# Performance work log

Measured on AMD Instinct MI355X. Metric: run time of the kernel, lower is better.

The kernel has to match this reference:

```python
import jax, jax.numpy as jnp
import numpy as np

B, BARS, BEATS, FRAC = 64, 16, 4, 8
IN_F = 10 * 47 * 2  # 940
LIN_OUT = 100
BEAT_H = 16
BAR_H = 32


def _p(key, shape, scale=0.05):
    return jax.random.normal(key, shape, dtype=jnp.float32) * scale


def setup_inputs() -> dict:
    key = jax.random.key(0)
    ks = jax.random.split(key, 16)
    return {
        "channels": jax.random.normal(ks[0], (B, BARS, BEATS, FRAC, 10, 2, 47), dtype=jnp.float32),
        "lin_w": _p(ks[1], (LIN_OUT, IN_F)),
        "lin_b": _p(ks[2], (LIN_OUT,)),
        # beats LSTM (unidirectional), PyTorch gate order i,f,g,o
        "b_wih": _p(ks[3], (4 * BEAT_H, LIN_OUT)),
        "b_whh": _p(ks[4], (4 * BEAT_H, BEAT_H)),
        "b_bih": _p(ks[5], (4 * BEAT_H,)),
        "b_bhh": _p(ks[6], (4 * BEAT_H,)),
        # bars LSTM, bidirectional: forward (f_) and reverse (r_) directions
        "f_wih": _p(ks[7], (4 * BAR_H, BEAT_H)),
        "f_whh": _p(ks[8], (4 * BAR_H, BAR_H)),
        "f_bih": _p(ks[9], (4 * BAR_H,)),
        "f_bhh": _p(ks[10], (4 * BAR_H,)),
        "r_wih": _p(ks[11], (4 * BAR_H, BEAT_H)),
        "r_whh": _p(ks[12], (4 * BAR_H, BAR_H)),
        "r_bih": _p(ks[13], (4 * BAR_H,)),
        "r_bhh": _p(ks[14], (4 * BAR_H,)),
    }


def lstm(x, wih, whh, bih, bhh):
    """PyTorch-semantics LSTM, batch_first. x: [N, T, F] -> h_seq [N, T, H]."""
    N = x.shape[0]
    H = whh.shape[1]
    # precompute input contribution for all timesteps
    xg = jnp.einsum('ntf,gf->ntg', x, wih) + (bih + bhh)  # [N, T, 4H]

    def step(carry, xt):
        h, c = carry
        gates = xt + h @ whh.T  # [N, 4H]
        i, f, g, o = jnp.split(gates, 4, axis=-1)
        c = jax.nn.sigmoid(f) * c + jax.nn.sigmoid(i) * jnp.tanh(g)
        h = jax.nn.sigmoid(o) * jnp.tanh(c)
        return (h, c), h

    h0 = jnp.zeros((N, H), x.dtype)
    _, hs = jax.lax.scan(step, (h0, h0), jnp.swapaxes(xg, 0, 1))  # [T, N, H]
    return jnp.swapaxes(hs, 0, 1)


def bilstm(x, f_wih, f_whh, f_bih, f_bhh, r_wih, r_whh, r_bih, r_bhh):
    fwd = lstm(x, f_wih, f_whh, f_bih, f_bhh)
    bwd = jnp.flip(lstm(jnp.flip(x, axis=1), r_wih, r_whh, r_bih, r_bhh), axis=1)
    return jnp.concatenate([fwd, bwd], axis=-1)


def reference(channels, lin_w, lin_b,
              b_wih, b_whh, b_bih, b_bhh,
              f_wih, f_whh, f_bih, f_bhh,
              r_wih, r_whh, r_bih, r_bhh):
    # channels: [B, bars, beats, frac, 10, 2, 47]
    x = jnp.swapaxes(channels, -1, -2)  # [..., 10, 47, 2]
    x = x.reshape(*x.shape[:4], IN_F)   # squash dims 4..6 -> 940
    x = jax.nn.relu(x @ lin_w.T + lin_b)  # [B, bars, beats, frac, 100]

    # Distributed depth=2: fold (B, bars, beats) into batch, seq over frac
    xb = x.reshape(B * BARS * BEATS, FRAC, LIN_OUT)
    beats = lstm(xb, b_wih, b_whh, b_bih, b_bhh)
    beats = beats.reshape(B, BARS, BEATS, FRAC, BEAT_H)

    # last fraction hidden state, then Distributed depth=1 over beats axis
    xl = beats[:, :, :, -1].reshape(B * BARS, BEATS, BEAT_H)
    bars = bilstm(xl, f_wih, f_whh, f_bih, f_bhh, r_wih, r_whh, r_bih, r_bhh)
    bars = bars.reshape(B, BARS, BEATS, 2 * BAR_H)
    return beats, bars
```

## Files before the change

kernel.cpp:

```cpp
#include <hip/hip_runtime.h>
#include <hip/hip_bf16.h>

typedef float f32x4 __attribute__((ext_vector_type(4)));
typedef short bf16x8 __attribute__((ext_vector_type(8)));

#define MFMA16(a, b, c) __builtin_amdgcn_mfma_f32_16x16x32_bf16(a, b, c, 0, 0, 0)

constexpr int K1  = 940;
constexpr int KP2 = 1024;
constexpr int NP  = 112;
constexpr int OSL = 136;

__device__ __forceinline__ float sigf(float x) { return 1.f / (1.f + __expf(-x)); }
__device__ __forceinline__ float tanhfast(float x) { return 2.f / (1.f + __expf(-2.f * x)) - 1.f; }

__device__ __forceinline__ short f2b(float x) {
  __hip_bfloat16 b = __float2bfloat16(x);
  return *reinterpret_cast<short*>(&b);
}

__global__ void prep_kernel(const float* __restrict__ lin_w,
                            const float* __restrict__ b_wih,
                            __hip_bfloat16* __restrict__ w2,
                            __hip_bfloat16* __restrict__ bw2) {
  int idx = blockIdx.x * 256 + threadIdx.x;
  if (idx < NP * KP2) {
    int n = idx >> 10, k = idx & 1023;
    float v = 0.f;
    if (n < 100 && k < K1) {
      int c10 = k / 94, rem = k - c10 * 94;
      int c2 = rem / 47, c47 = rem - c2 * 47;
      int f = c10 * 94 + c47 * 2 + c2;
      v = lin_w[n * K1 + f];
    }
    w2[idx] = __float2bfloat16(v);
  } else {
    int i2 = idx - NP * KP2;
    if (i2 < 64 * 128) {
      int g = i2 >> 7, k = i2 & 127;
      bw2[i2] = __float2bfloat16((k < 100) ? b_wih[g * 100 + k] : 0.f);
    }
  }
}

__global__ __launch_bounds__(512, 2)
void fused_encoder(const float* __restrict__ ch,
                   const __hip_bfloat16* __restrict__ w2,
                   const float* __restrict__ lin_b,
                   const __hip_bfloat16* __restrict__ bw2,
                   const float* __restrict__ bih,
                   const float* __restrict__ bhh,
                   const float* __restrict__ whh,
                   float* __restrict__ beats) {
  __shared__ float red[8 * 16 * NP];
  __shared__ __align__(16) __hip_bfloat16 out_s[64 * OSL];
  __shared__ float xg_s[64 * 65];
  const int tid = threadIdx.x;
  const int w = tid >> 6, lane = tid & 63;
  const int l16 = lane & 15, bq = lane >> 4;
  const int kbase = w * 128;

  bf16x8 breg[4][7];
#pragma unroll
  for (int s = 0; s < 4; ++s)
#pragma unroll
    for (int nt = 0; nt < 7; ++nt)
      breg[s][nt] = *reinterpret_cast<const bf16x8*>(
          &w2[(nt * 16 + l16) * KP2 + kbase + s * 32 + bq * 8]);

  const int mbase = blockIdx.x * 64;

  auto issueA = [&](int m0, float4* buf) {
    const float* ar = ch + (long)(m0 + l16) * K1 + kbase + bq * 8;
    if (w < 7) {
#pragma unroll
      for (int s = 0; s < 4; ++s) {
        buf[2 * s]     = *reinterpret_cast<const float4*>(ar + s * 32);
        buf[2 * s + 1] = *reinterpret_cast<const float4*>(ar + s * 32 + 4);
      }
    } else {
      buf[0] = *reinterpret_cast<const float4*>(ar);
      buf[1] = *reinterpret_cast<const float4*>(ar + 4);
      float t[8];
#pragma unroll
      for (int j = 0; j < 8; ++j) {
        int k = 928 + bq * 8 + j;
        t[j] = (k < K1) ? ar[32 + j] : 0.f;
      }
      buf[2] = float4{t[0], t[1], t[2], t[3]};
      buf[3] = float4{t[4], t[5], t[6], t[7]};
      buf[4] = buf[5] = buf[6] = buf[7] = float4{0.f, 0.f, 0.f, 0.f};
    }
  };

  float4 a0[8], a1[8];
  issueA(mbase, a0);

#pragma unroll
  for (int i = 0; i < 4; ++i) {
    float4* cur = (i & 1) ? a1 : a0;
    float4* nxt = (i & 1) ? a0 : a1;
    if (i < 3) issueA(mbase + (i + 1) * 16, nxt);

    f32x4 acc[7] = {};
#pragma unroll
    for (int s = 0; s < 4; ++s) {
      float4 lo = cur[2 * s], hi = cur[2 * s + 1];
      bf16x8 a = bf16x8{f2b(lo.x), f2b(lo.y), f2b(lo.z), f2b(lo.w),
                        f2b(hi.x), f2b(hi.y), f2b(hi.z), f2b(hi.w)};
#pragma unroll
      for (int nt = 0; nt < 7; ++nt) acc[nt] = MFMA16(a, breg[s][nt], acc[nt]);
    }

#pragma unroll
    for (int nt = 0; nt < 7; ++nt)
#pragma unroll
      for (int r = 0; r < 4; ++r)
        red[(w * 16 + bq * 4 + r) * NP + nt * 16 + l16] = acc[nt][r];
    __syncthreads();

    if (tid < 448) {
      const int col = tid % NP;
      const int rb = (tid / NP) * 4;
      const float bias = (col < 100) ? lin_b[col] : 0.f;
#pragma unroll
      for (int r = 0; r < 4; ++r) {
        float s = 0.f;
#pragma unroll
        for (int ww = 0; ww < 8; ++ww) s += red[(ww * 16 + rb + r) * NP + col];
        float v = fmaxf(s + bias, 0.f);
        out_s[(i * 16 + rb + r) * OSL + col] = __float2bfloat16((col < 100) ? v : 0.f);
      }
    } else {
      const int t2 = tid - 448;
      const int row = t2 >> 2, c0 = 112 + (t2 & 3) * 4;
#pragma unroll
      for (int q = 0; q < 4; ++q)
        out_s[(i * 16 + row) * OSL + c0 + q] = __float2bfloat16(0.f);
    }
    __syncthreads();
  }

  {
    const int rt = w >> 1, gt0 = (w & 1) * 2;
    bf16x8 av[4];
#pragma unroll
    for (int s = 0; s < 4; ++s)
      av[s] = *reinterpret_cast<const bf16x8*>(&out_s[(rt * 16 + l16) * OSL + s * 32 + bq * 8]);
    f32x4 xacc[2] = {{0.f, 0.f, 0.f, 0.f}, {0.f, 0.f, 0.f, 0.f}};
#pragma unroll
    for (int g2 = 0; g2 < 2; ++g2) {
      const int gt = gt0 + g2;
#pragma unroll
      for (int s = 0; s < 4; ++s) {
        bf16x8 b = *reinterpret_cast<const bf16x8*>(&bw2[(gt * 16 + l16) * 128 + s * 32 + bq * 8]);
        xacc[g2] = MFMA16(av[s], b, xacc[g2]);
      }
    }
#pragma unroll
    for (int g2 = 0; g2 < 2; ++g2) {
      const int gate = (gt0 + g2) * 16 + l16;
      const float bias = bih[gate] + bhh[gate];
#pragma unroll
      for (int r = 0; r < 4; ++r)
        xg_s[(rt * 16 + bq * 4 + r) * 65 + gate] = xacc[g2][r] + bias;
    }
  }
  __syncthreads();

  {
    const int cell = lane & 15;
    float wr[16];
#pragma unroll
    for (int u = 0; u < 16; ++u) wr[u] = whh[lane * 16 + u];
    float xv[8];
#pragma unroll
    for (int t = 0; t < 8; ++t) xv[t] = xg_s[(w * 8 + t) * 65 + lane];
    float h[16];
#pragma unroll
    for (int u = 0; u < 16; ++u) h[u] = 0.f;
    float c = 0.f;
    const int seq = blockIdx.x * 8 + w;
#pragma unroll
    for (int t = 0; t < 8; ++t) {
      float pre = xv[t];
#pragma unroll
      for (int u = 0; u < 16; ++u) pre += wr[u] * h[u];
      float act = (lane >= 32 && lane < 48) ? tanhfast(pre) : sigf(pre);
      float gi = __shfl(act, cell);
      float gf = __shfl(act, cell + 16);
      float gg = __shfl(act, cell + 32);
      float go = __shfl(act, cell + 48);
      c = gf * c + gi * gg;
      float hn = go * tanhfast(c);
#pragma unroll
      for (int u = 0; u < 16; ++u) h[u] = __shfl(hn, u);
      if (lane < 16) beats[seq * 128 + t * 16 + lane] = hn;
    }
  }
}

__global__ __launch_bounds__(256)
void bars_bilstm(const float* __restrict__ fwih, const float* __restrict__ fwhh,
                 const float* __restrict__ fbih, const float* __restrict__ fbhh,
                 const float* __restrict__ rwih, const float* __restrict__ rwhh,
                 const float* __restrict__ rbih, const float* __restrict__ rbhh,
                 const float* __restrict__ beats,
                 float* __restrict__ bars) {
  const int tid = threadIdx.x;
  const int dir = tid >> 7, g = tid & 127;
  const int n = blockIdx.x;
  const float* wih = dir ? rwih : fwih;
  const float* whh = dir ? rwhh : fwhh;
  const float bias = dir ? (rbih[g] + rbhh[g]) : (fbih[g] + fbhh[g]);
  float wi[16], wh[32];
#pragma unroll
  for (int u = 0; u < 16; ++u) wi[u] = wih[g * 16 + u];
#pragma unroll
  for (int u = 0; u < 32; ++u) wh[u] = whh[g * 32 + u];
  __shared__ float xbuf[2][16];
  __shared__ float hbuf[2][32];
  __shared__ float gact[2][128];
  float c = 0.f;
  if (g < 32) hbuf[dir][g] = 0.f;
  __syncthreads();
  for (int t = 0; t < 4; ++t) {
    const int tt = dir ? (3 - t) : t;
    if (g < 16) xbuf[dir][g] = beats[((n * 4 + tt) * 8 + 7) * 16 + g];
    __syncthreads();
    float pre = bias;
#pragma unroll
    for (int u = 0; u < 16; ++u) pre += wi[u] * xbuf[dir][u];
#pragma unroll
    for (int u = 0; u < 32; ++u) pre += wh[u] * hbuf[dir][u];
    gact[dir][g] = (g >= 64 && g < 96) ? tanhfast(pre) : sigf(pre);
    __syncthreads();
    if (g < 32) {
      c = gact[dir][32 + g] * c + gact[dir][g] * gact[dir][64 + g];
      float hn = gact[dir][96 + g] * tanhfast(c);
      hbuf[dir][g] = hn;
      bars[(n * 4 + tt) * 64 + dir * 32 + g] = hn;
    }
    __syncthreads();
  }
}

extern "C" void kernel_launch(void* const* d_in, const int* in_sizes, int n_in,
                              void* d_out, int out_size, void* d_ws, size_t ws_size,
                              hipStream_t stream) {
  const float* ch    = (const float*)d_in[0];
  const float* lin_w = (const float*)d_in[1];
  const float* lin_b = (const float*)d_in[2];
  const float* b_wih = (const float*)d_in[3];
  const float* b_whh = (const float*)d_in[4];
  const float* b_bih = (const float*)d_in[5];
  const float* b_bhh = (const float*)d_in[6];
  const float* f_wih = (const float*)d_in[7];
  const float* f_whh = (const float*)d_in[8];
  const float* f_bih = (const float*)d_in[9];
  const float* f_bhh = (const float*)d_in[10];
  const float* r_wih = (const float*)d_in[11];
  const float* r_whh = (const float*)d_in[12];
  const float* r_bih = (const float*)d_in[13];
  const float* r_bhh = (const float*)d_in[14];

  char* ws = (char*)d_ws;
  __hip_bfloat16* w2  = (__hip_bfloat16*)ws;
  __hip_bfloat16* bw2 = (__hip_bfloat16*)(ws + 229376);
  float*          out = (float*)d_out;

  prep_kernel<<<480, 256, 0, stream>>>(lin_w, b_wih, w2, bw2);
  fused_encoder<<<512, 512, 0, stream>>>(ch, w2, lin_b, bw2, b_bih, b_bhh,
                                         b_whh, out);
  bars_bilstm<<<1024, 256, 0, stream>>>(f_wih, f_whh, f_bih, f_bhh,
                                        r_wih, r_whh, r_bih, r_bhh,
                                        out, out + 524288);
}
```

Before: 236.7 us.

## Switch encoder GEMM from split-K across waves to per-wave row tiles

The fused encoder now runs 4 waves per block, and each wave owns 16 rows and walks the full K dimension itself. Previously 8 waves split K and reduced partial sums through a large shared-memory buffer with block barriers. B weights are now streamed from global (L2) with double buffering instead of being held in registers, and each wave runs two LSTM sequences interleaved. This removes the cross-wave reduction and most of the syncthreads, at the cost of re-reading the weight matrix per wave and a longer serial K loop per wave.

```diff
diff --git a/kernel.cpp b/kernel.cpp
--- a/kernel.cpp
+++ b/kernel.cpp
@@ -43,7 +43,7 @@
   }
 }
 
-__global__ __launch_bounds__(512, 2)
+__global__ __launch_bounds__(256, 2)
 void fused_encoder(const float* __restrict__ ch,
                    const __hip_bfloat16* __restrict__ w2,
                    const float* __restrict__ lin_b,
@@ -52,150 +52,154 @@
                    const float* __restrict__ bhh,
                    const float* __restrict__ whh,
                    float* __restrict__ beats) {
-  __shared__ float red[8 * 16 * NP];
   __shared__ __align__(16) __hip_bfloat16 out_s[64 * OSL];
   __shared__ float xg_s[64 * 65];
+
   const int tid = threadIdx.x;
   const int w = tid >> 6, lane = tid & 63;
   const int l16 = lane & 15, bq = lane >> 4;
-  const int kbase = w * 128;
-
-  bf16x8 breg[4][7];
-#pragma unroll
-  for (int s = 0; s < 4; ++s)
+
+  const int mbase = blockIdx.x * 64 + w * 16;
+  const float* ar = ch + (long)(mbase + l16) * K1 + bq * 8;
+
+  int bidx[7];
+#pragma unroll
+  for (int nt = 0; nt < 7; ++nt) bidx[nt] = (nt * 16 + l16) * KP2 + bq * 8;
+
+  float lb[7];
+#pragma unroll
+  for (int nt = 0; nt < 7; ++nt) {
+    int col = nt * 16 + l16;
+    lb[nt] = (col < 100) ? lin_b[col] : 0.f;
+  }
+
+  auto mk = [&](float4 lo, float4 hi) -> bf16x8 {
+    return bf16x8{f2b(lo.x), f2b(lo.y), f2b(lo.z), f2b(lo.w),
+                  f2b(hi.x), f2b(hi.y), f2b(hi.z), f2b(hi.w)};
+  };
+
+  f32x4 acc[7] = {};
+  float4 Ab[2][4];
+  bf16x8 Bb[2][7];
+
+  const float4 f40{0.f, 0.f, 0.f, 0.f};
+  auto ldA = [&](int c, float4* d) {
+    const float* p = ar + c * 64;
+    if (c < 14) {
+      d[0] = *reinterpret_cast<const float4*>(p);
+      d[1] = *reinterpret_cast<const float4*>(p + 4);
+      d[2] = *reinterpret_cast<const float4*>(p + 32);
+      d[3] = *reinterpret_cast<const float4*>(p + 36);
+    } else {
+      d[0] = *reinterpret_cast<const float4*>(p);
+      d[1] = *reinterpret_cast<const float4*>(p + 4);
+      d[2] = (bq <= 1) ? *reinterpret_cast<const float4*>(p + 32) : f40;
+      d[3] = (bq == 0) ? *reinterpret_cast<const float4*>(p + 36) : f40;
+    }
+  };
+  auto ldB = [&](int ks, bf16x8* d) {
 #pragma unroll
     for (int nt = 0; nt < 7; ++nt)
-      breg[s][nt] = *reinterpret_cast<const bf16x8*>(
-          &w2[(nt * 16 + l16) * KP2 + kbase + s * 32 + bq * 8]);
-
-  const int mbase = blockIdx.x * 64;
-
-  auto issueA = [&](int m0, float4* buf) {
-    const float* ar = ch + (long)(m0 + l16) * K1 + kbase + bq * 8;
-    if (w < 7) {
-#pragma unroll
-      for (int s = 0; s < 4; ++s) {
-        buf[2 * s]     = *reinterpret_cast<const float4*>(ar + s * 32);
-        buf[2 * s + 1] = *reinterpret_cast<const float4*>(ar + s * 32 + 4);
-      }
-    } else {
-      buf[0] = *reinterpret_cast<const float4*>(ar);
-      buf[1] = *reinterpret_cast<const float4*>(ar + 4);
-      float t[8];
-#pragma unroll
-      for (int j = 0; j < 8; ++j) {
-        int k = 928 + bq * 8 + j;
-        t[j] = (k < K1) ? ar[32 + j] : 0.f;
-      }
-      buf[2] = float4{t[0], t[1], t[2], t[3]};
-      buf[3] = float4{t[4], t[5], t[6], t[7]};
-      buf[4] = buf[5] = buf[6] = buf[7] = float4{0.f, 0.f, 0.f, 0.f};
-    }
+      d[nt] = *reinterpret_cast<const bf16x8*>(&w2[bidx[nt] + ks * 32]);
   };
 
-  float4 a0[8], a1[8];
-  issueA(mbase, a0);
-
-#pragma unroll
-  for (int i = 0; i < 4; ++i) {
-    float4* cur = (i & 1) ? a1 : a0;
-    float4* nxt = (i & 1) ? a0 : a1;
-    if (i < 3) issueA(mbase + (i + 1) * 16, nxt);
-
-    f32x4 acc[7] = {};
-#pragma unroll
-    for (int s = 0; s < 4; ++s) {
-      float4 lo = cur[2 * s], hi = cur[2 * s + 1];
-      bf16x8 a = bf16x8{f2b(lo.x), f2b(lo.y), f2b(lo.z), f2b(lo.w),
-                        f2b(hi.x), f2b(hi.y), f2b(hi.z), f2b(hi.w)};
-#pragma unroll
-      for (int nt = 0; nt < 7; ++nt) acc[nt] = MFMA16(a, breg[s][nt], acc[nt]);
-    }
-
-#pragma unroll
-    for (int nt = 0; nt < 7; ++nt)
-#pragma unroll
-      for (int r = 0; r < 4; ++r)
-        red[(w * 16 + bq * 4 + r) * NP + nt * 16 + l16] = acc[nt][r];
-    __syncthreads();
-
-    if (tid < 448) {
-      const int col = tid % NP;
-      const int rb = (tid / NP) * 4;
-      const float bias = (col < 100) ? lin_b[col] : 0.f;
-#pragma unroll
-      for (int r = 0; r < 4; ++r) {
-        float s = 0.f;
-#pragma unroll
-        for (int ww = 0; ww < 8; ++ww) s += red[(ww * 16 + rb + r) * NP + col];
-        float v = fmaxf(s + bias, 0.f);
-        out_s[(i * 16 + rb + r) * OSL + col] = __float2bfloat16((col < 100) ? v : 0.f);
-      }
-    } else {
-      const int t2 = tid - 448;
-      const int row = t2 >> 2, c0 = 112 + (t2 & 3) * 4;
-#pragma unroll
-      for (int q = 0; q < 4; ++q)
-        out_s[(i * 16 + row) * OSL + c0 + q] = __float2bfloat16(0.f);
-    }
-    __syncthreads();
-  }
+  ldA(0, Ab[0]);
+  ldB(0, Bb[0]);
+  ldB(1, Bb[1]);
+#pragma unroll
+  for (int c = 0; c < 15; ++c) {
+    float4* A = Ab[c & 1];
+    if (c < 14) ldA(c + 1, Ab[(c + 1) & 1]);
+    {
+      bf16x8 a = mk(A[0], A[1]);
+#pragma unroll
+      for (int nt = 0; nt < 7; ++nt) acc[nt] = MFMA16(a, Bb[0][nt], acc[nt]);
+    }
+    if (c < 14) ldB(2 * c + 2, Bb[0]);
+    {
+      bf16x8 a = mk(A[2], A[3]);
+#pragma unroll
+      for (int nt = 0; nt < 7; ++nt) acc[nt] = MFMA16(a, Bb[1][nt], acc[nt]);
+    }
+    if (c < 14) ldB(2 * c + 3, Bb[1]);
+  }
+
+#pragma unroll
+  for (int nt = 0; nt < 7; ++nt) {
+    const int col = nt * 16 + l16;
+#pragma unroll
+    for (int r = 0; r < 4; ++r) {
+      float v = fmaxf(acc[nt][r] + lb[nt], 0.f);
+      out_s[(w * 16 + bq * 4 + r) * OSL + col] = __float2bfloat16((col < 100) ? v : 0.f);
+    }
+  }
+#pragma unroll
+  for (int r = 0; r < 4; ++r)
+    out_s[(w * 16 + bq * 4 + r) * OSL + 112 + l16] = __float2bfloat16(0.f);
 
   {
-    const int rt = w >> 1, gt0 = (w & 1) * 2;
     bf16x8 av[4];
 #pragma unroll
     for (int s = 0; s < 4; ++s)
-      av[s] = *reinterpret_cast<const bf16x8*>(&out_s[(rt * 16 + l16) * OSL + s * 32 + bq * 8]);
-    f32x4 xacc[2] = {{0.f, 0.f, 0.f, 0.f}, {0.f, 0.f, 0.f, 0.f}};
-#pragma unroll
-    for (int g2 = 0; g2 < 2; ++g2) {
-      const int gt = gt0 + g2;
+      av[s] = *reinterpret_cast<const bf16x8*>(&out_s[(w * 16 + l16) * OSL + s * 32 + bq * 8]);
+    f32x4 xacc[4] = {};
+#pragma unroll
+    for (int gt = 0; gt < 4; ++gt) {
 #pragma unroll
       for (int s = 0; s < 4; ++s) {
         bf16x8 b = *reinterpret_cast<const bf16x8*>(&bw2[(gt * 16 + l16) * 128 + s * 32 + bq * 8]);
-        xacc[g2] = MFMA16(av[s], b, xacc[g2]);
+        xacc[gt] = MFMA16(av[s], b, xacc[gt]);
       }
     }
 #pragma unroll
-    for (int g2 = 0; g2 < 2; ++g2) {
-      const int gate = (gt0 + g2) * 16 + l16;
+    for (int gt = 0; gt < 4; ++gt) {
+      const int gate = gt * 16 + l16;
       const float bias = bih[gate] + bhh[gate];
 #pragma unroll
       for (int r = 0; r < 4; ++r)
-        xg_s[(rt * 16 + bq * 4 + r) * 65 + gate] = xacc[g2][r] + bias;
-    }
-  }
-  __syncthreads();
+        xg_s[(w * 16 + bq * 4 + r) * 65 + gate] = xacc[gt][r] + bias;
+    }
+  }
 
   {
     const int cell = lane & 15;
     float wr[16];
 #pragma unroll
     for (int u = 0; u < 16; ++u) wr[u] = whh[lane * 16 + u];
-    float xv[8];
-#pragma unroll
-    for (int t = 0; t < 8; ++t) xv[t] = xg_s[(w * 8 + t) * 65 + lane];
-    float h[16];
-#pragma unroll
-    for (int u = 0; u < 16; ++u) h[u] = 0.f;
-    float c = 0.f;
-    const int seq = blockIdx.x * 8 + w;
+    float xv0[8], xv1[8];
 #pragma unroll
     for (int t = 0; t < 8; ++t) {
-      float pre = xv[t];
-#pragma unroll
-      for (int u = 0; u < 16; ++u) pre += wr[u] * h[u];
-      float act = (lane >= 32 && lane < 48) ? tanhfast(pre) : sigf(pre);
-      float gi = __shfl(act, cell);
-      float gf = __shfl(act, cell + 16);
-      float gg = __shfl(act, cell + 32);
-      float go = __shfl(act, cell + 48);
-      c = gf * c + gi * gg;
-      float hn = go * tanhfast(c);
-#pragma unroll
-      for (int u = 0; u < 16; ++u) h[u] = __shfl(hn, u);
-      if (lane < 16) beats[seq * 128 + t * 16 + lane] = hn;
+      xv0[t] = xg_s[(w * 16 + t) * 65 + lane];
+      xv1[t] = xg_s[(w * 16 + 8 + t) * 65 + lane];
+    }
+    float h0[16], h1[16];
+#pragma unroll
+    for (int u = 0; u < 16; ++u) { h0[u] = 0.f; h1[u] = 0.f; }
+    float c0 = 0.f, c1 = 0.f;
+    const long sg0 = (long)blockIdx.x * 8 + 2 * w;
+    const long sg1 = sg0 + 1;
+#pragma unroll
+    for (int t = 0; t < 8; ++t) {
+      float p0 = xv0[t], p1 = xv1[t];
+#pragma unroll
+      for (int u = 0; u < 16; ++u) { p0 += wr[u] * h0[u]; p1 += wr[u] * h1[u]; }
+      const bool istanh = (lane >= 32 && lane < 48);
+      float a0 = istanh ? tanhfast(p0) : sigf(p0);
+      float a1 = istanh ? tanhfast(p1) : sigf(p1);
+      float gi0 = __shfl(a0, cell),      gi1 = __shfl(a1, cell);
+      float gf0 = __shfl(a0, cell + 16), gf1 = __shfl(a1, cell + 16);
+      float gg0 = __shfl(a0, cell + 32), gg1 = __shfl(a1, cell + 32);
+      float go0 = __shfl(a0, cell + 48), go1 = __shfl(a1, cell + 48);
+      c0 = gf0 * c0 + gi0 * gg0;
+      c1 = gf1 * c1 + gi1 * gg1;
+      float hn0 = go0 * tanhfast(c0);
+      float hn1 = go1 * tanhfast(c1);
+#pragma unroll
+      for (int u = 0; u < 16; ++u) { h0[u] = __shfl(hn0, u); h1[u] = __shfl(hn1, u); }
+      if (lane < 16) {
+        beats[sg0 * 128 + t * 16 + lane] = hn0;
+        beats[sg1 * 128 + t * 16 + lane] = hn1;
+      }
     }
   }
 }
@@ -270,7 +274,7 @@
   float*          out = (float*)d_out;
 
   prep_kernel<<<480, 256, 0, stream>>>(lin_w, b_wih, w2, bw2);
-  fused_encoder<<<512, 512, 0, stream>>>(ch, w2, lin_b, bw2, b_bih, b_bhh,
+  fused_encoder<<<512, 256, 0, stream>>>(ch, w2, lin_b, bw2, b_bih, b_bhh,
                                          b_whh, out);
   bars_bilstm<<<1024, 256, 0, stream>>>(f_wih, f_whh, f_bih, f_bhh,
                                         r_wih, r_whh, r_bih, r_bhh,
```

After: 264.9 us. 11.9% more time.
